# Performance work log

Hardware: AMD Instinct MI355X
Metric: run time of the kernel (lower is better)

## Reference

```python
import jax, jax.numpy as jnp
import numpy as np


def setup_inputs() -> dict:
    key = jax.random.key(0)
    k1, k2 = jax.random.split(key)
    B, S, H = 32, 4096, 1024
    query = jax.random.normal(k1, (B, H), dtype=jnp.float32)
    values = jax.random.normal(k2, (B, S, H), dtype=jnp.float32)
    scale = jnp.ones((S, 1), dtype=jnp.float32)  # learned per-position scale (use_scale=True)
    return {"query": query, "values": values, "scale": scale}


def reference(query, values, scale):
    # score = values @ query^T over hidden dim -> [B, S]
    score = jnp.einsum('bsh,bh->bs', values, query)
    score = score * scale[:, 0]               # broadcast (S,) over batch
    attn = jax.nn.softmax(score, axis=1)       # softmax over source positions
    # context = sum_s attn[b,s] * values[b,s,:] -> [B, H]
    context = jnp.einsum('bs,bsh->bh', attn, values)
    return context
```

## Files before the change

### kernel.cpp

```cpp
#include <hip/hip_runtime.h>
#include <math.h>

#define BATCH 32
#define SEQ   4096
#define HD    1024

template <int CPB>
__global__ __launch_bounds__(256)
void luong_pass1(const float* __restrict__ q,
                 const float* __restrict__ v,
                 const float* __restrict__ scale,
                 float* __restrict__ ws_acc,
                 float* __restrict__ ws_m,
                 float* __restrict__ ws_l)
{
    constexpr int ROWS = SEQ / CPB;
    constexpr int RPW  = ROWS / 4;
    const int blk  = blockIdx.x;
    const int b    = blk / CPB;
    const int ch   = blk % CPB;
    const int tid  = threadIdx.x;
    const int wid  = tid >> 6;
    const int lane = tid & 63;

    const float4* q4 = (const float4*)(q + (size_t)b * HD);
    float4 qf[4];
#pragma unroll
    for (int k = 0; k < 4; ++k) qf[k] = q4[k * 64 + lane];

    float  m = -INFINITY, l = 0.f;
    float4 acc[4];
#pragma unroll
    for (int k = 0; k < 4; ++k) acc[k] = make_float4(0.f, 0.f, 0.f, 0.f);

    const int s0 = ch * ROWS + wid * RPW;
    for (int r = 0; r < RPW; ++r) {
        const int s = s0 + r;
        const float4* v4 = (const float4*)(v + ((size_t)b * SEQ + s) * HD);
        float4 vf[4];
#pragma unroll
        for (int k = 0; k < 4; ++k) vf[k] = v4[k * 64 + lane];

        float d = 0.f;
#pragma unroll
        for (int k = 0; k < 4; ++k)
            d += vf[k].x * qf[k].x + vf[k].y * qf[k].y
               + vf[k].z * qf[k].z + vf[k].w * qf[k].w;
#pragma unroll
        for (int off = 32; off >= 1; off >>= 1)
            d += __shfl_xor(d, off, 64);

        const float sc = d * scale[s];
        if (sc <= m) {
            const float p = __expf(sc - m);
            l += p;
#pragma unroll
            for (int k = 0; k < 4; ++k) {
                acc[k].x += p * vf[k].x;  acc[k].y += p * vf[k].y;
                acc[k].z += p * vf[k].z;  acc[k].w += p * vf[k].w;
            }
        } else {
            const float f = __expf(m - sc);
            l = l * f + 1.f;
#pragma unroll
            for (int k = 0; k < 4; ++k) {
                acc[k].x = acc[k].x * f + vf[k].x;
                acc[k].y = acc[k].y * f + vf[k].y;
                acc[k].z = acc[k].z * f + vf[k].z;
                acc[k].w = acc[k].w * f + vf[k].w;
            }
            m = sc;
        }
    }

    __shared__ float lds_m[4], lds_l[4];
    __shared__ float lds_acc[4][HD];
    if (lane == 0) { lds_m[wid] = m; lds_l[wid] = l; }
    __syncthreads();
    const float M  = fmaxf(fmaxf(lds_m[0], lds_m[1]), fmaxf(lds_m[2], lds_m[3]));
    const float fw = __expf(m - M);
    float4* la = (float4*)lds_acc[wid];
#pragma unroll
    for (int k = 0; k < 4; ++k) {
        float4 t;
        t.x = acc[k].x * fw; t.y = acc[k].y * fw;
        t.z = acc[k].z * fw; t.w = acc[k].w * fw;
        la[k * 64 + lane] = t;
    }
    __syncthreads();

    float lblk = 0.f;
#pragma unroll
    for (int w = 0; w < 4; ++w) lblk += lds_l[w] * __expf(lds_m[w] - M);

    const float4 a0 = ((const float4*)lds_acc[0])[tid];
    const float4 a1 = ((const float4*)lds_acc[1])[tid];
    const float4 a2 = ((const float4*)lds_acc[2])[tid];
    const float4 a3 = ((const float4*)lds_acc[3])[tid];
    float4 sum;
    sum.x = a0.x + a1.x + a2.x + a3.x;
    sum.y = a0.y + a1.y + a2.y + a3.y;
    sum.z = a0.z + a1.z + a2.z + a3.z;
    sum.w = a0.w + a1.w + a2.w + a3.w;
    ((float4*)(ws_acc + (size_t)blk * HD))[tid] = sum;
    if (tid == 0) { ws_m[blk] = M; ws_l[blk] = lblk; }
}

template <int CPB>
__global__ __launch_bounds__(256)
void luong_pass2(const float* __restrict__ ws_acc,
                 const float* __restrict__ ws_m,
                 const float* __restrict__ ws_l,
                 float* __restrict__ out)
{
    const int b   = blockIdx.x;
    const int tid = threadIdx.x;

    float M = -INFINITY;
#pragma unroll
    for (int i = 0; i < CPB; ++i) M = fmaxf(M, ws_m[b * CPB + i]);
    float T = 0.f;
#pragma unroll
    for (int i = 0; i < CPB; ++i) T += ws_l[b * CPB + i] * __expf(ws_m[b * CPB + i] - M);
    const float invT = 1.f / T;

    float4 sum = make_float4(0.f, 0.f, 0.f, 0.f);
#pragma unroll
    for (int i = 0; i < CPB; ++i) {
        const float wi = __expf(ws_m[b * CPB + i] - M) * invT;
        const float4 a = ((const float4*)(ws_acc + (size_t)(b * CPB + i) * HD))[tid];
        sum.x += wi * a.x; sum.y += wi * a.y;
        sum.z += wi * a.z; sum.w += wi * a.w;
    }
    ((float4*)(out + (size_t)b * HD))[tid] = sum;
}

template <int CPB>
static void launch_impl(const float* q, const float* v, const float* scale,
                        float* out, float* ws, hipStream_t stream)
{
    const int NB = BATCH * CPB;
    float* ws_acc = ws;
    float* ws_m   = ws + (size_t)NB * HD;
    float* ws_l   = ws_m + NB;
    luong_pass1<CPB><<<NB, 256, 0, stream>>>(q, v, scale, ws_acc, ws_m, ws_l);
    luong_pass2<CPB><<<BATCH, 256, 0, stream>>>(ws_acc, ws_m, ws_l, out);
}

extern "C" void kernel_launch(void* const* d_in, const int* in_sizes, int n_in,
                              void* d_out, int out_size, void* d_ws, size_t ws_size,
                              hipStream_t stream)
{
    const float* q     = (const float*)d_in[0];
    const float* v     = (const float*)d_in[1];
    const float* scale = (const float*)d_in[2];
    float* out = (float*)d_out;
    float* ws  = (float*)d_ws;

    int cpb = 32;
    while (cpb > 1 &&
           (size_t)BATCH * cpb * (HD + 2) * sizeof(float) > ws_size)
        cpb >>= 1;

    switch (cpb) {
        case 32: launch_impl<32>(q, v, scale, out, ws, stream); break;
        case 16: launch_impl<16>(q, v, scale, out, ws, stream); break;
        case 8:  launch_impl<8>(q, v, scale, out, ws, stream); break;
        case 4:  launch_impl<4>(q, v, scale, out, ws, stream); break;
        case 2:  launch_impl<2>(q, v, scale, out, ws, stream); break;
        default: launch_impl<1>(q, v, scale, out, ws, stream); break;
    }
}
```

Before: 111.2 us.

## Software-pipeline row loads in pairs with double-buffered registers in pass1

Pass1 now handles two value rows per step. It keeps two register buffers so the next pair's global loads are issued before the current pair is processed, overlapping memory latency with the dot products and online-softmax updates. It also merges the two rows' softmax rescale into one branch and adds a minimum-occupancy hint to launch bounds. The trade-off is higher register pressure, which the occupancy hint may force into spills.

```diff
diff --git a/kernel.cpp b/kernel.cpp
--- a/kernel.cpp
+++ b/kernel.cpp
@@ -5,8 +5,77 @@
 #define SEQ   4096
 #define HD    1024
 
+
+struct RowPair {
+    float4 a[4];
+    float4 b[4];
+    float  sa, sb;
+};
+
+__device__ __forceinline__ void load_pair(const float* __restrict__ vb,
+                                          const float* __restrict__ scale,
+                                          int s, int lane, RowPair& rp)
+{
+    const float4* v4a = (const float4*)(vb + (size_t)s * HD);
+    const float4* v4b = (const float4*)(vb + (size_t)(s + 1) * HD);
+#pragma unroll
+    for (int k = 0; k < 4; ++k) {
+        rp.a[k] = v4a[k * 64 + lane];
+        rp.b[k] = v4b[k * 64 + lane];
+    }
+    rp.sa = scale[s];
+    rp.sb = scale[s + 1];
+}
+
+__device__ __forceinline__ void process_pair(const RowPair& rp,
+                                             const float4* __restrict__ qf,
+                                             float& m, float& l, float4* acc)
+{
+    float d0 = 0.f, d1 = 0.f;
+#pragma unroll
+    for (int k = 0; k < 4; ++k) {
+        d0 += rp.a[k].x * qf[k].x + rp.a[k].y * qf[k].y
+            + rp.a[k].z * qf[k].z + rp.a[k].w * qf[k].w;
+        d1 += rp.b[k].x * qf[k].x + rp.b[k].y * qf[k].y
+            + rp.b[k].z * qf[k].z + rp.b[k].w * qf[k].w;
+    }
+#pragma unroll
+    for (int off = 32; off >= 1; off >>= 1) {
+        d0 += __shfl_xor(d0, off, 64);
+        d1 += __shfl_xor(d1, off, 64);
+    }
+    const float sc0 = d0 * rp.sa;
+    const float sc1 = d1 * rp.sb;
+    const float mx  = fmaxf(sc0, sc1);
+    if (mx <= m) {
+        const float p0 = __expf(sc0 - m);
+        const float p1 = __expf(sc1 - m);
+        l += p0 + p1;
+#pragma unroll
+        for (int k = 0; k < 4; ++k) {
+            acc[k].x += p0 * rp.a[k].x + p1 * rp.b[k].x;
+            acc[k].y += p0 * rp.a[k].y + p1 * rp.b[k].y;
+            acc[k].z += p0 * rp.a[k].z + p1 * rp.b[k].z;
+            acc[k].w += p0 * rp.a[k].w + p1 * rp.b[k].w;
+        }
+    } else {
+        const float f  = __expf(m - mx);
+        const float p0 = __expf(sc0 - mx);
+        const float p1 = __expf(sc1 - mx);
+        l = l * f + p0 + p1;
+#pragma unroll
+        for (int k = 0; k < 4; ++k) {
+            acc[k].x = acc[k].x * f + p0 * rp.a[k].x + p1 * rp.b[k].x;
+            acc[k].y = acc[k].y * f + p0 * rp.a[k].y + p1 * rp.b[k].y;
+            acc[k].z = acc[k].z * f + p0 * rp.a[k].z + p1 * rp.b[k].z;
+            acc[k].w = acc[k].w * f + p0 * rp.a[k].w + p1 * rp.b[k].w;
+        }
+        m = mx;
+    }
+}
+
 template <int CPB>
-__global__ __launch_bounds__(256)
+__global__ __launch_bounds__(256, 4)
 void luong_pass1(const float* __restrict__ q,
                  const float* __restrict__ v,
                  const float* __restrict__ scale,
@@ -16,6 +85,9 @@
 {
     constexpr int ROWS = SEQ / CPB;
     constexpr int RPW  = ROWS / 4;
+    constexpr int NP   = RPW / 2;
+    static_assert(NP >= 2 && (NP % 2) == 0, "pipeline needs even NP>=2");
+
     const int blk  = blockIdx.x;
     const int b    = blk / CPB;
     const int ch   = blk % CPB;
@@ -34,44 +106,20 @@
     for (int k = 0; k < 4; ++k) acc[k] = make_float4(0.f, 0.f, 0.f, 0.f);
 
     const int s0 = ch * ROWS + wid * RPW;
-    for (int r = 0; r < RPW; ++r) {
-        const int s = s0 + r;
-        const float4* v4 = (const float4*)(v + ((size_t)b * SEQ + s) * HD);
-        float4 vf[4];
-#pragma unroll
-        for (int k = 0; k < 4; ++k) vf[k] = v4[k * 64 + lane];
-
-        float d = 0.f;
-#pragma unroll
-        for (int k = 0; k < 4; ++k)
-            d += vf[k].x * qf[k].x + vf[k].y * qf[k].y
-               + vf[k].z * qf[k].z + vf[k].w * qf[k].w;
-#pragma unroll
-        for (int off = 32; off >= 1; off >>= 1)
-            d += __shfl_xor(d, off, 64);
-
-        const float sc = d * scale[s];
-        if (sc <= m) {
-            const float p = __expf(sc - m);
-            l += p;
-#pragma unroll
-            for (int k = 0; k < 4; ++k) {
-                acc[k].x += p * vf[k].x;  acc[k].y += p * vf[k].y;
-                acc[k].z += p * vf[k].z;  acc[k].w += p * vf[k].w;
-            }
-        } else {
-            const float f = __expf(m - sc);
-            l = l * f + 1.f;
-#pragma unroll
-            for (int k = 0; k < 4; ++k) {
-                acc[k].x = acc[k].x * f + vf[k].x;
-                acc[k].y = acc[k].y * f + vf[k].y;
-                acc[k].z = acc[k].z * f + vf[k].z;
-                acc[k].w = acc[k].w * f + vf[k].w;
-            }
-            m = sc;
-        }
-    }
+    const float* vb = v + (size_t)b * SEQ * HD;
+
+    RowPair A, B;
+    load_pair(vb, scale, s0, lane, A);
+#pragma unroll 1
+    for (int i = 0; i < NP - 2; i += 2) {
+        load_pair(vb, scale, s0 + 2 * (i + 1), lane, B);
+        process_pair(A, qf, m, l, acc);
+        load_pair(vb, scale, s0 + 2 * (i + 2), lane, A);
+        process_pair(B, qf, m, l, acc);
+    }
+    load_pair(vb, scale, s0 + 2 * (NP - 1), lane, B);
+    process_pair(A, qf, m, l, acc);
+    process_pair(B, qf, m, l, acc);
 
     __shared__ float lds_m[4], lds_l[4];
     __shared__ float lds_acc[4][HD];
```

Result: slower. 138.1 us (+24.2%).

## Double-buffer value row loads with nontemporal hints and branchless online softmax

Applied to the files above, without the earlier changes.

Restructures the pass-1 row loop so the next row of values is loaded into a second register buffer while the current row is processed, overlapping global-load latency with the dot-product reduction and accumulation. Loads now use nontemporal builtins, since values are streamed once. The divergent online-softmax branch becomes a branchless max/rescale form that computes two exps per row. Per-row scale values are preloaded once per wave and broadcast with a shuffle. These changes raise register pressure and add extra exp work per row, and the kernel is likely bandwidth-bound already.

```diff
diff --git a/kernel.cpp b/kernel.cpp
--- a/kernel.cpp
+++ b/kernel.cpp
@@ -4,6 +4,49 @@
 #define BATCH 32
 #define SEQ   4096
 #define HD    1024
+
+typedef float floatx4 __attribute__((ext_vector_type(4)));
+
+
+__device__ __forceinline__ void load_row(const float* __restrict__ vb,
+                                         int s, int lane, float4* vf)
+{
+    const floatx4* v4 = (const floatx4*)(vb + (size_t)s * HD);
+#pragma unroll
+    for (int k = 0; k < 4; ++k) {
+        floatx4 t = __builtin_nontemporal_load(&v4[k * 64 + lane]);
+        vf[k] = make_float4(t.x, t.y, t.z, t.w);
+    }
+}
+
+__device__ __forceinline__ void process_row(const float4* vf,
+                                            const float4* qf,
+                                            float scale_r,
+                                            float& m, float& l, float4* acc)
+{
+    float d = 0.f;
+#pragma unroll
+    for (int k = 0; k < 4; ++k)
+        d += vf[k].x * qf[k].x + vf[k].y * qf[k].y
+           + vf[k].z * qf[k].z + vf[k].w * qf[k].w;
+#pragma unroll
+    for (int off = 32; off >= 1; off >>= 1)
+        d += __shfl_xor(d, off, 64);
+
+    const float sc = d * scale_r;
+    const float mn = fmaxf(m, sc);
+    const float f  = __expf(m - mn);
+    const float p  = __expf(sc - mn);
+    l = l * f + p;
+#pragma unroll
+    for (int k = 0; k < 4; ++k) {
+        acc[k].x = acc[k].x * f + p * vf[k].x;
+        acc[k].y = acc[k].y * f + p * vf[k].y;
+        acc[k].z = acc[k].z * f + p * vf[k].z;
+        acc[k].w = acc[k].w * f + p * vf[k].w;
+    }
+    m = mn;
+}
 
 template <int CPB>
 __global__ __launch_bounds__(256)
@@ -16,6 +59,8 @@
 {
     constexpr int ROWS = SEQ / CPB;
     constexpr int RPW  = ROWS / 4;
+    static_assert(RPW >= 4 && (RPW % 2) == 0, "pipeline shape");
+
     const int blk  = blockIdx.x;
     const int b    = blk / CPB;
     const int ch   = blk % CPB;
@@ -28,50 +73,35 @@
 #pragma unroll
     for (int k = 0; k < 4; ++k) qf[k] = q4[k * 64 + lane];
 
+    const int s0 = ch * ROWS + wid * RPW;
+    const float* vb = v + (size_t)b * SEQ * HD;
+
+    float scl = 0.f;
+    if constexpr (RPW <= 64) {
+        scl = (lane < RPW) ? scale[s0 + lane] : 0.f;
+    }
+    auto get_scale = [&](int r) -> float {
+        if constexpr (RPW <= 64) return __shfl(scl, r, 64);
+        else                     return scale[s0 + r];
+    };
+
     float  m = -INFINITY, l = 0.f;
     float4 acc[4];
 #pragma unroll
     for (int k = 0; k < 4; ++k) acc[k] = make_float4(0.f, 0.f, 0.f, 0.f);
 
-    const int s0 = ch * ROWS + wid * RPW;
-    for (int r = 0; r < RPW; ++r) {
-        const int s = s0 + r;
-        const float4* v4 = (const float4*)(v + ((size_t)b * SEQ + s) * HD);
-        float4 vf[4];
-#pragma unroll
-        for (int k = 0; k < 4; ++k) vf[k] = v4[k * 64 + lane];
-
-        float d = 0.f;
-#pragma unroll
-        for (int k = 0; k < 4; ++k)
-            d += vf[k].x * qf[k].x + vf[k].y * qf[k].y
-               + vf[k].z * qf[k].z + vf[k].w * qf[k].w;
-#pragma unroll
-        for (int off = 32; off >= 1; off >>= 1)
-            d += __shfl_xor(d, off, 64);
-
-        const float sc = d * scale[s];
-        if (sc <= m) {
-            const float p = __expf(sc - m);
-            l += p;
-#pragma unroll
-            for (int k = 0; k < 4; ++k) {
-                acc[k].x += p * vf[k].x;  acc[k].y += p * vf[k].y;
-                acc[k].z += p * vf[k].z;  acc[k].w += p * vf[k].w;
-            }
-        } else {
-            const float f = __expf(m - sc);
-            l = l * f + 1.f;
-#pragma unroll
-            for (int k = 0; k < 4; ++k) {
-                acc[k].x = acc[k].x * f + vf[k].x;
-                acc[k].y = acc[k].y * f + vf[k].y;
-                acc[k].z = acc[k].z * f + vf[k].z;
-                acc[k].w = acc[k].w * f + vf[k].w;
-            }
-            m = sc;
-        }
-    }
+    float4 va[4], vbuf[4];
+    load_row(vb, s0, lane, va);
+#pragma unroll 1
+    for (int r = 0; r < RPW - 2; r += 2) {
+        load_row(vb, s0 + r + 1, lane, vbuf);
+        process_row(va, qf, get_scale(r), m, l, acc);
+        load_row(vb, s0 + r + 2, lane, va);
+        process_row(vbuf, qf, get_scale(r + 1), m, l, acc);
+    }
+    load_row(vb, s0 + RPW - 1, lane, vbuf);
+    process_row(va, qf, get_scale(RPW - 2), m, l, acc);
+    process_row(vbuf, qf, get_scale(RPW - 1), m, l, acc);
 
     __shared__ float lds_m[4], lds_l[4];
     __shared__ float lds_acc[4][HD];
```

Result: faster. 101.1 us (-9.1%).
